# Kernel optimization log

Measured on AMD Instinct MI355X. Metric: run time of the kernel, lower is better.

## Reference

```python
import jax, jax.numpy as jnp
import numpy as np

N = 50000
E = 800000
H = 96
NUM_IN = 11
PE_DIM = 24
NUM_OUT = 1
NUM_LAYERS = 4
NUM_GRAPHS = 256


def _linear_params(key, d_in, d_out):
    k1, k2 = jax.random.split(key)
    bound = 1.0 / np.sqrt(d_in)
    w = jax.random.uniform(k1, (d_in, d_out), jnp.float32, -bound, bound)
    b = jax.random.uniform(k2, (d_out,), jnp.float32, -bound, bound)
    return w, b


def setup_inputs() -> dict:
    key = jax.random.key(0)
    ks = jax.random.split(key, 32)
    x = jax.random.normal(ks[0], (N, NUM_IN), jnp.float32)
    pos = jax.random.normal(ks[1], (N, 3), jnp.float32)
    pe = jax.random.normal(ks[2], (N, PE_DIM), jnp.float32)
    edge_index = jax.random.randint(ks[3], (2, E), 0, N, jnp.int64)
    batch = jnp.sort(jax.random.randint(ks[4], (N,), 0, NUM_GRAPHS, jnp.int64))
    embed_w1, embed_b1 = _linear_params(ks[5], NUM_IN + PE_DIM, H)
    embed_w2, embed_b2 = _linear_params(ks[6], H, H)
    # per-layer stacked params
    msg_w1 = []; msg_b1 = []; msg_w2 = []; msg_b2 = []
    upd_w1 = []; upd_b1 = []; upd_w2 = []; upd_b2 = []
    for l in range(NUM_LAYERS):
        w, b = _linear_params(ks[7 + l], 2 * H + 1, H); msg_w1.append(w); msg_b1.append(b)
        w, b = _linear_params(ks[11 + l], H, H); msg_w2.append(w); msg_b2.append(b)
        w, b = _linear_params(ks[15 + l], 2 * H, H); upd_w1.append(w); upd_b1.append(b)
        w, b = _linear_params(ks[19 + l], H, H); upd_w2.append(w); upd_b2.append(b)
    pre_w1, pre_b1 = _linear_params(ks[23], H, H)
    pre_w2, pre_b2 = _linear_params(ks[24], H, H)
    ro_w1, ro_b1 = _linear_params(ks[25], H, H)
    ro_w2, ro_b2 = _linear_params(ks[26], H, NUM_OUT)
    return {
        'x': x, 'pos': pos, 'pe': pe, 'edge_index': edge_index, 'batch': batch,
        'embed_w1': embed_w1, 'embed_b1': embed_b1, 'embed_w2': embed_w2, 'embed_b2': embed_b2,
        'msg_w1': jnp.stack(msg_w1), 'msg_b1': jnp.stack(msg_b1),
        'msg_w2': jnp.stack(msg_w2), 'msg_b2': jnp.stack(msg_b2),
        'upd_w1': jnp.stack(upd_w1), 'upd_b1': jnp.stack(upd_b1),
        'upd_w2': jnp.stack(upd_w2), 'upd_b2': jnp.stack(upd_b2),
        'pre_w1': pre_w1, 'pre_b1': pre_b1, 'pre_w2': pre_w2, 'pre_b2': pre_b2,
        'ro_w1': ro_w1, 'ro_b1': ro_b1, 'ro_w2': ro_w2, 'ro_b2': ro_b2,
    }


def _egnn_forward(x, pos, pe, edge_index, batch,
                  embed_w1, embed_b1, embed_w2, embed_b2,
                  msg_w1, msg_b1, msg_w2, msg_b2,
                  upd_w1, upd_b1, upd_w2, upd_b2,
                  pre_w1, pre_b1, pre_w2, pre_b2,
                  ro_w1, ro_b1, ro_w2, ro_b2):
    silu = jax.nn.silu
    send, rec = edge_index[0], edge_index[1]
    h = jnp.concatenate([x, pe], axis=-1)
    h = silu(h @ embed_w1 + embed_b1) @ embed_w2 + embed_b2  # [N,H]
    dist = jnp.linalg.norm(pos[send] - pos[rec], axis=1)[:, None]  # [E,1]
    for l in range(NUM_LAYERS):
        state = jnp.concatenate([h[send], h[rec], dist], axis=1)  # [E,2H+1]
        msg = silu(silu(state @ msg_w1[l] + msg_b1[l]) @ msg_w2[l] + msg_b2[l])  # [E,H]
        aggr = jax.ops.segment_sum(msg, rec, num_segments=h.shape[0])  # [N,H]
        upd_in = jnp.concatenate([h, aggr], axis=1)
        update = silu(upd_in @ upd_w1[l] + upd_b1[l]) @ upd_w2[l] + upd_b2[l]
        h = h + update
    h = silu(h @ pre_w1 + pre_b1) @ pre_w2 + pre_b2
    pooled = jax.ops.segment_sum(h, batch, num_segments=NUM_GRAPHS)  # [G,H]
    out = silu(pooled @ ro_w1 + ro_b1) @ ro_w2 + ro_b2  # [G,1]
    return jnp.squeeze(out)


def reference(x, pos, pe, edge_index, batch,
              embed_w1, embed_b1, embed_w2, embed_b2,
              msg_w1, msg_b1, msg_w2, msg_b2,
              upd_w1, upd_b1, upd_w2, upd_b2,
              pre_w1, pre_b1, pre_w2, pre_b2,
              ro_w1, ro_b1, ro_w2, ro_b2):
    return _egnn_forward(x, pos, pe, edge_index, batch,
                         embed_w1, embed_b1, embed_w2, embed_b2,
                         msg_w1, msg_b1, msg_w2, msg_b2,
                         upd_w1, upd_b1, upd_w2, upd_b2,
                         pre_w1, pre_b1, pre_w2, pre_b2,
                         ro_w1, ro_b1, ro_w2, ro_b2)
```

## Files before the change

### kernel.cpp

```cpp
#include <hip/hip_runtime.h>
#include <hip/hip_bf16.h>

#define HDIM 96
#define TILE 128
#define NTILE 64

typedef __attribute__((ext_vector_type(8))) short  short8;
typedef __attribute__((ext_vector_type(4))) short  short4v;
typedef __attribute__((ext_vector_type(4))) float  float4v;
typedef __attribute__((ext_vector_type(2))) float  float2v;
typedef __attribute__((ext_vector_type(4))) unsigned int uint4v;

static __device__ __forceinline__ short f2bf(float f){
    unsigned u = __float_as_uint(f);
    return (short)((u + 0x8000u) >> 16);
}
static __device__ __forceinline__ float bf2f(short s){
    unsigned u = ((unsigned)(unsigned short)s) << 16;
    return __uint_as_float(u);
}
static __device__ __forceinline__ float silu_f(float v){
    return v * __builtin_amdgcn_rcpf(1.0f + __expf(-v));
}

struct SwJob { const float* src; int ck; int ks; int ksrc; };
struct SwTable { SwJob j[22]; };

__global__ __launch_bounds__(256) void swizzle_all(SwTable T, const float* __restrict__ msg_w1,
                                                   short* __restrict__ dst, short* __restrict__ dst2,
                                                   int total1, int total2){
    int gid = blockIdx.x*256 + threadIdx.x;
    if (gid < total1) {
        int ksg = gid / 3072;
        int e   = gid % 3072;
        const float* src = T.j[0].src; int k0 = 0, ksrc = 0;
        #pragma unroll
        for (int jj = 0; jj < 22; ++jj){
            int s = T.j[jj].ck;
            if (ksg >= s && ksg < s + T.j[jj].ks){ src = T.j[jj].src; k0 = (ksg - s)*32; ksrc = T.j[jj].ksrc; }
        }
        int nt   = e >> 9;
        int rem  = e & 511;
        int lane = rem >> 3;
        int jx   = rem & 7;
        int k = k0 + ((lane >> 4) << 3) + jx;
        int f = nt*16 + (lane & 15);
        float v = (k < ksrc) ? src[(size_t)k*HDIM + f] : 0.0f;
        dst[gid] = f2bf(v);
    } else if (gid < total1 + total2) {
        int g2 = gid - total1;
        int layer = g2 / 18432;
        int e     = g2 % 18432;
        int ksg = e / 6144;
        int rem = e % 6144;
        int nt   = rem >> 9;
        int r2   = rem & 511;
        int lane = r2 >> 3;
        int jx   = r2 & 7;
        int k = ksg*32 + ((lane >> 4) << 3) + jx;
        int f = nt*16 + (lane & 15);
        int row = (f < 96) ? k : (96 + k);
        int col = (f < 96) ? f : (f - 96);
        dst2[g2] = f2bf(msg_w1[(size_t)layer*193*96 + (size_t)row*96 + col]);
    }
}

__global__ __launch_bounds__(256) void hist_kernel(const int* __restrict__ rec, int* __restrict__ deg, int E){
    int e = blockIdx.x*256 + threadIdx.x;
    if (e < E) atomicAdd(&deg[rec[e]], 1);
}

__global__ __launch_bounds__(256) void scan_part(const int* __restrict__ deg, int* __restrict__ part, int N){
    __shared__ int red[256];
    const int t = threadIdx.x;
    int base = blockIdx.x*1024;
    int s = 0;
    #pragma unroll
    for (int j=0;j<4;j++){ int i = base + j*256 + t; s += (i<N)?deg[i]:0; }
    red[t]=s; __syncthreads();
    #pragma unroll
    for (int off=128; off>0; off>>=1){ if (t<off) red[t]+=red[t+off]; __syncthreads(); }
    if (t==0) part[blockIdx.x]=red[0];
}
__global__ __launch_bounds__(256) void scan_top(int* __restrict__ part, int nb){
    __shared__ int buf[256];
    const int t = threadIdx.x;
    int v = (t < nb) ? part[t] : 0;
    buf[t] = v;
    __syncthreads();
    #pragma unroll
    for (int off=1; off<256; off<<=1){
        int u = (t>=off)?buf[t-off]:0;
        __syncthreads();
        buf[t] += u;
        __syncthreads();
    }
    if (t < nb) part[t] = buf[t] - v;
}
__global__ __launch_bounds__(256) void scan_final(const int* __restrict__ deg, const int* __restrict__ part,
                                                  int* __restrict__ cur, int N){
    __shared__ int tsum[256];
    const int t = threadIdx.x;
    int i0 = blockIdx.x*1024 + t*4;
    int a0 = (i0+0<N)?deg[i0+0]:0;
    int a1 = (i0+1<N)?deg[i0+1]:0;
    int a2 = (i0+2<N)?deg[i0+2]:0;
    int a3 = (i0+3<N)?deg[i0+3]:0;
    int s = a0+a1+a2+a3;
    tsum[t]=s; __syncthreads();
    #pragma unroll
    for (int off=1; off<256; off<<=1){
        int u = (t>=off)?tsum[t-off]:0;
        __syncthreads();
        tsum[t]+=u;
        __syncthreads();
    }
    int excl = tsum[t]-s + part[blockIdx.x];
    if (i0+0<N) cur[i0+0]=excl;
    if (i0+1<N) cur[i0+1]=excl+a0;
    if (i0+2<N) cur[i0+2]=excl+a0+a1;
    if (i0+3<N) cur[i0+3]=excl+a0+a1+a2;
}

__global__ __launch_bounds__(256) void scatter_kernel(
    const int* __restrict__ send, const int* __restrict__ rec, const float* __restrict__ pos,
    int* __restrict__ cur, int2* __restrict__ sd_s, int* __restrict__ rec_s, int E)
{
    int e = blockIdx.x*256 + threadIdx.x;
    if (e >= E) return;
    int s = send[e], r = rec[e];
    int p = atomicAdd(&cur[r], 1);
    float dx = pos[3*s]   - pos[3*r];
    float dy = pos[3*s+1] - pos[3*r+1];
    float dz = pos[3*s+2] - pos[3*r+2];
    float d = sqrtf(dx*dx + dy*dy + dz*dz);
    sd_s[p] = make_int2(s, __float_as_int(d));
    rec_s[p] = r;
}

__global__ __launch_bounds__(256,5) void edge_kernel(
    const short* __restrict__ SR,
    const int2* __restrict__ sd_s, const int* __restrict__ rec_s,
    const float* __restrict__ w1r192,
    const short* __restrict__ w2sw, const float* __restrict__ b2,
    float* __restrict__ aggr, float* __restrict__ stageA, float* __restrict__ stageB, int E)
{
    __shared__ short msgS[TILE*104];
    __shared__ int   recS[TILE];
    __shared__ int   startIdxS[TILE+1];
    __shared__ int   wcntS[2];
    const int t  = threadIdx.x;
    const int e0 = blockIdx.x * TILE;
    const int lane = t & 63;
    const int wv   = t >> 6;
    const int e_lo = wv * 32;
    const int col  = lane & 15;
    const int quad = lane >> 4;
    const int frow = quad * 4;
    const float4v fzero = {0.f,0.f,0.f,0.f};

    int se[2], re[2]; float dd[2];
    #pragma unroll
    for (int et=0; et<2; ++et){
        int ec = e0 + e_lo + et*16 + col; if (ec >= E) ec = E - 1;
        int2 sd = sd_s[ec];
        se[et] = sd.x; dd[et] = __int_as_float(sd.y);
        re[et] = rec_s[ec];
    }
    short8 Sv[2][3], Rv[2][3];
    #pragma unroll
    for (int et=0; et<2; ++et)
      #pragma unroll
      for (int ks=0; ks<3; ++ks){
        int f0 = ks*32 + quad*8;
        Sv[et][ks] = *(const short8*)(SR + (size_t)se[et]*192 + f0);
        Rv[et][ks] = *(const short8*)(SR + (size_t)re[et]*192 + 96 + f0);
      }

    int myRec = 0;
    bool flag = false;
    if (t < TILE) {
        int e = e0 + t; if (e >= E) e = E - 1;
        myRec = rec_s[e];
        recS[t] = myRec;
        int ep = e0 + t - 1; if (ep >= E) ep = E - 1;
        flag = (t == 0) || (myRec != rec_s[ep]);
    }
    unsigned long long bmask = __ballot(flag ? 1 : 0);
    int pre = __popcll(bmask & ((1ull << (t & 63)) - 1ull));
    if (t < TILE && (t & 63) == 0) wcntS[t >> 6] = __popcll(bmask);

    const bool firstB = (e0 > 0) && (rec_s[e0-1] == rec_s[e0]);
    const bool lastB  = (e0 + TILE < E) && (rec_s[e0 + TILE] == rec_s[(e0+TILE-1 < E)? e0+TILE-1 : E-1]);

    __syncthreads();

    if (flag) startIdxS[pre + ((t >> 6) ? wcntS[0] : 0)] = t;
    if (t == 0) startIdxS[wcntS[0] + wcntS[1]] = TILE;

    short8 frag[2][3];
    #pragma unroll
    for (int et=0; et<2; ++et){
        float d = dd[et];
        #pragma unroll
        for (int ks=0; ks<3; ++ks){
            int f0 = ks*32 + quad*8;
            float4v wa = *(const float4v*)(w1r192 + f0);
            float4v wb = *(const float4v*)(w1r192 + f0 + 4);
            short8 S8 = Sv[et][ks], R8 = Rv[et][ks];
            short8 fr;
            #pragma unroll
            for (int j=0;j<8;j++){
                float w = (j<4) ? wa[j] : wb[j-4];
                float v = bf2f(S8[j]) + bf2f(R8[j]) + d*w;
                fr[j] = f2bf(silu_f(v));
            }
            frag[et][ks] = fr;
        }
    }

    float4v acc2[2][6];
    #pragma unroll
    for (int i=0;i<2;i++)
      #pragma unroll
      for (int n=0;n<6;n++) acc2[i][n] = fzero;

    const short8* w2f = (const short8*)w2sw;
    #pragma unroll
    for (int ks = 0; ks < 3; ++ks) {
        #pragma unroll
        for (int mt = 0; mt < 6; ++mt) {
            short8 a = w2f[(ks*6+mt)*64 + lane];
            acc2[0][mt] = __builtin_amdgcn_mfma_f32_16x16x32_bf16(a, frag[0][ks], acc2[0][mt], 0, 0, 0);
            acc2[1][mt] = __builtin_amdgcn_mfma_f32_16x16x32_bf16(a, frag[1][ks], acc2[1][mt], 0, 0, 0);
        }
    }
    float4v b2v[6];
    #pragma unroll
    for (int mt=0; mt<6; ++mt) b2v[mt] = *(const float4v*)(b2 + mt*16 + frow);

    #pragma unroll
    for (int et=0; et<2; ++et){
        int e = e_lo + et*16 + col;
        bool valid = (e0 + e) < E;
        #pragma unroll
        for (int mt=0; mt<6; ++mt){
            short4v sv;
            #pragma unroll
            for (int r=0;r<4;r++){
                float u = silu_f(acc2[et][mt][r] + b2v[mt][r]);
                sv[r] = f2bf(valid ? u : 0.0f);
            }
            *(short4v*)(msgS + e*104 + mt*16 + frow) = sv;
        }
    }
    __syncthreads();

    const int nseg = wcntS[0] + wcntS[1];
    const int items = nseg * 12;
    for (int item = t; item < items; item += 256){
        int s  = item / 12;
        int fg = item - s*12;
        int r0 = startIdxS[s], r1 = startIdxS[s+1];
        float2v s01 = {0.f,0.f}, s23 = {0.f,0.f}, s45 = {0.f,0.f}, s67 = {0.f,0.f};
        for (int r = r0; r < r1; ++r){
            const unsigned* pp = (const unsigned*)(msgS + r*104 + fg*8);
            unsigned p0 = pp[0], p1 = pp[1], p2 = pp[2], p3 = pp[3];
            float2v a0 = { __uint_as_float(p0 << 16), __uint_as_float(p0 & 0xffff0000u) };
            float2v a1 = { __uint_as_float(p1 << 16), __uint_as_float(p1 & 0xffff0000u) };
            float2v a2 = { __uint_as_float(p2 << 16), __uint_as_float(p2 & 0xffff0000u) };
            float2v a3 = { __uint_as_float(p3 << 16), __uint_as_float(p3 & 0xffff0000u) };
            s01 += a0; s23 += a1; s45 += a2; s67 += a3;
        }
        int node = recS[r0];
        float* dstp;
        if (s == 0 && firstB)            dstp = stageB + (size_t)node*HDIM + fg*8;
        else if (s == nseg-1 && lastB)   dstp = stageA + (size_t)node*HDIM + fg*8;
        else                             dstp = aggr   + (size_t)node*HDIM + fg*8;
        float4v lo = {s01[0], s01[1], s23[0], s23[1]};
        float4v hi = {s45[0], s45[1], s67[0], s67[1]};
        *(float4v*)(dstp)     = lo;
        *(float4v*)(dstp + 4) = hi;
    }
}

__global__ __launch_bounds__(128,3) void update_kernel(
    short* __restrict__ hbf, const float* __restrict__ aggr,
    const float* __restrict__ stageA, const float* __restrict__ stageB,
    const int* __restrict__ deg, const int* __restrict__ cur,
    const short* __restrict__ w1sw, const float* __restrict__ b1,
    const short* __restrict__ w2sw, const float* __restrict__ b2,
    const short* __restrict__ w1sr_next, const float* __restrict__ msgb1_next,
    short* __restrict__ SR,
    const short* __restrict__ pw1, const float* __restrict__ pb1,
    const short* __restrict__ pw2, const float* __restrict__ pb2,
    const int* __restrict__ batch, float* __restrict__ pooled, int N)
{
    __shared__ short stateS[NTILE*208];
    __shared__ int   batchS[NTILE];
    __shared__ int   startIdxS[NTILE+1];
    __shared__ int   nsegS;
    const int t  = threadIdx.x;
    const int n0 = blockIdx.x * NTILE;

    #pragma unroll
    for (int it = 0; it < 12; ++it) {
        int q = it*128 + t;
        int c = q % 24;
        int i = q / 24;
        int node = n0 + i;
        if (c < 12) {
            uint4v v = {0u,0u,0u,0u};
            if (node < N) v = *(const uint4v*)(hbf + (size_t)node*HDIM + c*8);
            *(uint4v*)(stateS + i*200 + c*8) = v;
        } else {
            int cc = c - 12;
            short8 s8 = {0,0,0,0,0,0,0,0};
            if (node < N) {
                int dg = deg[node];
                int en = cur[node];
                int st = en - dg;
                bool bnd = (dg > 0) && (st/TILE != (en-1)/TILE);
                float4v a0, a1;
                if (bnd) {
                    size_t b = (size_t)node*HDIM + cc*8;
                    a0 = *(const float4v*)(stageA + b)     + *(const float4v*)(stageB + b);
                    a1 = *(const float4v*)(stageA + b + 4) + *(const float4v*)(stageB + b + 4);
                } else {
                    a0 = *(const float4v*)(aggr + (size_t)node*HDIM + cc*8);
                    a1 = *(const float4v*)(aggr + (size_t)node*HDIM + cc*8 + 4);
                }
                s8[0]=f2bf(a0[0]); s8[1]=f2bf(a0[1]); s8[2]=f2bf(a0[2]); s8[3]=f2bf(a0[3]);
                s8[4]=f2bf(a1[0]); s8[5]=f2bf(a1[1]); s8[6]=f2bf(a1[2]); s8[7]=f2bf(a1[3]);
            }
            *(short8*)(stateS + i*200 + HDIM + cc*8) = s8;
        }
    }
    __syncthreads();

    const int lane = t & 63;
    const int wv   = t >> 6;
    const int e_lo = wv * 32;
    const int col  = lane & 15;
    const int quad = lane >> 4;
    const int koff = quad * 8;
    const int frow = quad * 4;
    const float4v fzero = {0.f,0.f,0.f,0.f};

    float4v acc[2][6];
    #pragma unroll
    for (int i=0;i<2;i++)
      #pragma unroll
      for (int n=0;n<6;n++) acc[i][n] = fzero;

    const short8* w1f = (const short8*)w1sw;
    #pragma unroll
    for (int ks = 0; ks < 6; ++ks) {
        short8 bb0 = *(const short8*)(stateS + (e_lo+col)*200    + ks*32 + koff);
        short8 bb1 = *(const short8*)(stateS + (e_lo+16+col)*200 + ks*32 + koff);
        #pragma unroll
        for (int mt = 0; mt < 6; ++mt) {
            short8 a = w1f[(ks*6+mt)*64 + lane];
            acc[0][mt] = __builtin_amdgcn_mfma_f32_16x16x32_bf16(a, bb0, acc[0][mt], 0, 0, 0);
            acc[1][mt] = __builtin_amdgcn_mfma_f32_16x16x32_bf16(a, bb1, acc[1][mt], 0, 0, 0);
        }
    }
    float4v b1v[6];
    #pragma unroll
    for (int mt=0; mt<6; ++mt) b1v[mt] = *(const float4v*)(b1 + mt*16 + frow);
    __syncthreads();

    short* t1S = stateS;
    #pragma unroll
    for (int et=0; et<2; ++et){
        int e = e_lo + et*16 + col;
        #pragma unroll
        for (int mt=0; mt<6; ++mt){
            short4v sv;
            #pragma unroll
            for (int r=0;r<4;r++) sv[r] = f2bf(silu_f(acc[et][mt][r] + b1v[mt][r]));
            *(short4v*)(t1S + e*104 + mt*16 + frow) = sv;
        }
    }
    __syncthreads();

    float4v acc2[2][6];
    #pragma unroll
    for (int i=0;i<2;i++)
      #pragma unroll
      for (int n=0;n<6;n++) acc2[i][n] = fzero;

    const short8* w2f = (const short8*)w2sw;
    #pragma unroll
    for (int ks = 0; ks < 3; ++ks) {
        short8 bb0 = *(const short8*)(t1S + (e_lo+col)*104    + ks*32 + koff);
        short8 bb1 = *(const short8*)(t1S + (e_lo+16+col)*104 + ks*32 + koff);
        #pragma unroll
        for (int mt = 0; mt < 6; ++mt) {
            short8 a = w2f[(ks*6+mt)*64 + lane];
            acc2[0][mt] = __builtin_amdgcn_mfma_f32_16x16x32_bf16(a, bb0, acc2[0][mt], 0, 0, 0);
            acc2[1][mt] = __builtin_amdgcn_mfma_f32_16x16x32_bf16(a, bb1, acc2[1][mt], 0, 0, 0);
        }
    }
    float4v b2v[6];
    #pragma unroll
    for (int mt=0; mt<6; ++mt) b2v[mt] = *(const float4v*)(b2 + mt*16 + frow);
    __syncthreads();

    #pragma unroll
    for (int et=0; et<2; ++et){
        int erow = e_lo + et*16 + col;
        int node = n0 + erow;
        bool valid = node < N;
        size_t base = (size_t)node*HDIM;
        #pragma unroll
        for (int mt=0; mt<6; ++mt){
            int f0 = mt*16 + frow;
            short4v ov = {0,0,0,0};
            if (valid) ov = *(const short4v*)(hbf + base + f0);
            float4v o;
            #pragma unroll
            for (int r=0;r<4;r++) o[r] = bf2f(ov[r]) + acc2[et][mt][r] + b2v[mt][r];
            short4v sv = {f2bf(o[0]), f2bf(o[1]), f2bf(o[2]), f2bf(o[3])};
            if (valid) *(short4v*)(hbf + base + f0) = sv;
            *(short4v*)(stateS + erow*104 + f0) = sv;
        }
    }

    if (w1sr_next) {
        __syncthreads();
        float4v accS[2][12];
        #pragma unroll
        for (int i=0;i<2;i++)
          #pragma unroll
          for (int n=0;n<12;n++) accS[i][n] = fzero;

        const short8* wsf = (const short8*)w1sr_next;
        #pragma unroll
        for (int ks = 0; ks < 3; ++ks) {
            short8 bb0 = *(const short8*)(stateS + (e_lo+col)*104    + ks*32 + koff);
            short8 bb1 = *(const short8*)(stateS + (e_lo+16+col)*104 + ks*32 + koff);
            #pragma unroll
            for (int mt = 0; mt < 12; ++mt) {
                short8 a = wsf[(ks*12+mt)*64 + lane];
                accS[0][mt] = __builtin_amdgcn_mfma_f32_16x16x32_bf16(a, bb0, accS[0][mt], 0, 0, 0);
                accS[1][mt] = __builtin_amdgcn_mfma_f32_16x16x32_bf16(a, bb1, accS[1][mt], 0, 0, 0);
            }
        }
        float4v bnv[6];
        #pragma unroll
        for (int mt=0; mt<6; ++mt) bnv[mt] = *(const float4v*)(msgb1_next + mt*16 + frow);

        #pragma unroll
        for (int et=0; et<2; ++et){
            int node = n0 + e_lo + et*16 + col;
            if (node < N) {
                size_t sbase = (size_t)node*192;
                #pragma unroll
                for (int mt=0; mt<12; ++mt){
                    float4v o = accS[et][mt];
                    if (mt < 6) { o[0]+=bnv[mt][0]; o[1]+=bnv[mt][1]; o[2]+=bnv[mt][2]; o[3]+=bnv[mt][3]; }
                    short4v sv = {f2bf(o[0]), f2bf(o[1]), f2bf(o[2]), f2bf(o[3])};
                    *(short4v*)(SR + sbase + mt*16 + frow) = sv;
                }
            }
        }
    } else if (pw1) {
        if (t < NTILE) {
            int node = n0 + t;
            batchS[t] = batch[node < N ? node : N-1];
        }
        __syncthreads();

        bool flag = false;
        if (t < NTILE) flag = (t == 0) || (batchS[t] != batchS[t-1]);
        unsigned long long bm = __ballot(flag ? 1 : 0);
        if (t < NTILE) {
            int pre = __popcll(bm & ((1ull << t) - 1ull));
            if (flag) startIdxS[pre] = t;
            if (t == 0) nsegS = __popcll(bm);
        }

        float4v accp[2][6];
        #pragma unroll
        for (int i=0;i<2;i++)
          #pragma unroll
          for (int n=0;n<6;n++) accp[i][n] = fzero;

        const short8* pw1f = (const short8*)pw1;
        #pragma unroll
        for (int ks = 0; ks < 3; ++ks) {
            short8 bb0 = *(const short8*)(stateS + (e_lo+col)*104    + ks*32 + koff);
            short8 bb1 = *(const short8*)(stateS + (e_lo+16+col)*104 + ks*32 + koff);
            #pragma unroll
            for (int mt = 0; mt < 6; ++mt) {
                short8 a = pw1f[(ks*6+mt)*64 + lane];
                accp[0][mt] = __builtin_amdgcn_mfma_f32_16x16x32_bf16(a, bb0, accp[0][mt], 0, 0, 0);
                accp[1][mt] = __builtin_amdgcn_mfma_f32_16x16x32_bf16(a, bb1, accp[1][mt], 0, 0, 0);
            }
        }
        float4v pb1v[6];
        #pragma unroll
        for (int mt=0; mt<6; ++mt) pb1v[mt] = *(const float4v*)(pb1 + mt*16 + frow);

        short* t1p = stateS + NTILE*104;
        #pragma unroll
        for (int et=0; et<2; ++et){
            int e = e_lo + et*16 + col;
            #pragma unroll
            for (int mt=0; mt<6; ++mt){
                short4v sv;
                #pragma unroll
                for (int r=0;r<4;r++) sv[r] = f2bf(silu_f(accp[et][mt][r] + pb1v[mt][r]));
                *(short4v*)(t1p + e*104 + mt*16 + frow) = sv;
            }
        }
        __syncthreads();

        float4v accq[2][6];
        #pragma unroll
        for (int i=0;i<2;i++)
          #pragma unroll
          for (int n=0;n<6;n++) accq[i][n] = fzero;

        const short8* pw2f = (const short8*)pw2;
        #pragma unroll
        for (int ks = 0; ks < 3; ++ks) {
            short8 bb0 = *(const short8*)(t1p + (e_lo+col)*104    + ks*32 + koff);
            short8 bb1 = *(const short8*)(t1p + (e_lo+16+col)*104 + ks*32 + koff);
            #pragma unroll
            for (int mt = 0; mt < 6; ++mt) {
                short8 a = pw2f[(ks*6+mt)*64 + lane];
                accq[0][mt] = __builtin_amdgcn_mfma_f32_16x16x32_bf16(a, bb0, accq[0][mt], 0, 0, 0);
                accq[1][mt] = __builtin_amdgcn_mfma_f32_16x16x32_bf16(a, bb1, accq[1][mt], 0, 0, 0);
            }
        }
        float4v pb2v[6];
        #pragma unroll
        for (int mt=0; mt<6; ++mt) pb2v[mt] = *(const float4v*)(pb2 + mt*16 + frow);
        __syncthreads();

        float* msgS = (float*)stateS;
        #pragma unroll
        for (int et=0; et<2; ++et){
            int e = e_lo + et*16 + col;
            bool valid = (n0 + e) < N;
            #pragma unroll
            for (int mt=0; mt<6; ++mt){
                float4v v;
                #pragma unroll
                for (int r=0;r<4;r++){
                    float u = accq[et][mt][r] + pb2v[mt][r];
                    v[r] = valid ? u : 0.0f;
                }
                *(float4v*)(msgS + e*100 + mt*16 + frow) = v;
            }
        }
        __syncthreads();

        const int nseg = nsegS;
        if (t == 0) startIdxS[nseg] = NTILE;
        __syncthreads();

        const int items = nseg * 24;
        for (int item = t; item < items; item += 128){
            int s  = item / 24;
            int fg = item - s*24;
            int r0 = startIdxS[s], r1 = startIdxS[s+1];
            float4v sum = fzero;
            for (int r = r0; r < r1; ++r) sum += *(const float4v*)(msgS + r*100 + fg*4);
            float* dstp = pooled + (size_t)batchS[r0]*HDIM + fg*4;
            atomicAdd(dstp+0, sum[0]);
            atomicAdd(dstp+1, sum[1]);
            atomicAdd(dstp+2, sum[2]);
            atomicAdd(dstp+3, sum[3]);
        }
    }
}

__global__ __launch_bounds__(128,3) void embed_kernel(
    const float* __restrict__ x, const float* __restrict__ pe,
    const short* __restrict__ w1sw, const float* __restrict__ b1,
    const short* __restrict__ w2sw, const float* __restrict__ b2,
    short* __restrict__ hbf,
    const short* __restrict__ w1sr0, const float* __restrict__ msgb1_0,
    short* __restrict__ SR, int N)
{
    __shared__ short stateS[NTILE*72];
    __shared__ short t1S[NTILE*104];
    const int t  = threadIdx.x;
    const int n0 = blockIdx.x * NTILE;

    if (t < NTILE) {
        int node = n0 + t;
        short* row = stateS + t*72;
        if (node < N) {
            #pragma unroll
            for (int j=0;j<11;j++) row[j]    = f2bf(x[(size_t)node*11 + j]);
            #pragma unroll
            for (int j=0;j<24;j++) row[11+j] = f2bf(pe[(size_t)node*24 + j]);
            #pragma unroll
            for (int j=35;j<64;j++) row[j] = 0;
        } else {
            #pragma unroll
            for (int j=0;j<64;j++) row[j] = 0;
        }
    }
    __syncthreads();

    const int lane = t & 63;
    const int wv   = t >> 6;
    const int e_lo = wv * 32;
    const int col  = lane & 15;
    const int quad = lane >> 4;
    const int koff = quad * 8;
    const int frow = quad * 4;
    const float4v fzero = {0.f,0.f,0.f,0.f};

    float4v acc[2][6];
    #pragma unroll
    for (int i=0;i<2;i++)
      #pragma unroll
      for (int n=0;n<6;n++) acc[i][n] = fzero;

    const short8* w1f = (const short8*)w1sw;
    #pragma unroll
    for (int ks = 0; ks < 2; ++ks) {
        short8 bb0 = *(const short8*)(stateS + (e_lo+col)*72    + ks*32 + koff);
        short8 bb1 = *(const short8*)(stateS + (e_lo+16+col)*72 + ks*32 + koff);
        #pragma unroll
        for (int mt = 0; mt < 6; ++mt) {
            short8 a = w1f[(ks*6+mt)*64 + lane];
            acc[0][mt] = __builtin_amdgcn_mfma_f32_16x16x32_bf16(a, bb0, acc[0][mt], 0, 0, 0);
            acc[1][mt] = __builtin_amdgcn_mfma_f32_16x16x32_bf16(a, bb1, acc[1][mt], 0, 0, 0);
        }
    }
    float4v b1v[6];
    #pragma unroll
    for (int mt=0; mt<6; ++mt) b1v[mt] = *(const float4v*)(b1 + mt*16 + frow);

    #pragma unroll
    for (int et=0; et<2; ++et){
        int e = e_lo + et*16 + col;
        #pragma unroll
        for (int mt=0; mt<6; ++mt){
            short4v sv;
            #pragma unroll
            for (int r=0;r<4;r++) sv[r] = f2bf(silu_f(acc[et][mt][r] + b1v[mt][r]));
            *(short4v*)(t1S + e*104 + mt*16 + frow) = sv;
        }
    }
    __syncthreads();

    float4v acc2[2][6];
    #pragma unroll
    for (int i=0;i<2;i++)
      #pragma unroll
      for (int n=0;n<6;n++) acc2[i][n] = fzero;

    const short8* w2f = (const short8*)w2sw;
    #pragma unroll
    for (int ks = 0; ks < 3; ++ks) {
        short8 bb0 = *(const short8*)(t1S + (e_lo+col)*104    + ks*32 + koff);
        short8 bb1 = *(const short8*)(t1S + (e_lo+16+col)*104 + ks*32 + koff);
        #pragma unroll
        for (int mt = 0; mt < 6; ++mt) {
            short8 a = w2f[(ks*6+mt)*64 + lane];
            acc2[0][mt] = __builtin_amdgcn_mfma_f32_16x16x32_bf16(a, bb0, acc2[0][mt], 0, 0, 0);
            acc2[1][mt] = __builtin_amdgcn_mfma_f32_16x16x32_bf16(a, bb1, acc2[1][mt], 0, 0, 0);
        }
    }
    float4v b2v[6];
    #pragma unroll
    for (int mt=0; mt<6; ++mt) b2v[mt] = *(const float4v*)(b2 + mt*16 + frow);
    __syncthreads();

    #pragma unroll
    for (int et=0; et<2; ++et){
        int erow = e_lo + et*16 + col;
        int node = n0 + erow;
        bool valid = node < N;
        size_t base = (size_t)node*HDIM;
        #pragma unroll
        for (int mt=0; mt<6; ++mt){
            int f0 = mt*16 + frow;
            float4v o;
            #pragma unroll
            for (int r=0;r<4;r++) o[r] = acc2[et][mt][r] + b2v[mt][r];
            short4v sv = {f2bf(o[0]), f2bf(o[1]), f2bf(o[2]), f2bf(o[3])};
            if (valid) *(short4v*)(hbf + base + f0) = sv;
            *(short4v*)(t1S + erow*104 + f0) = sv;
        }
    }
    __syncthreads();

    float4v accS[2][12];
    #pragma unroll
    for (int i=0;i<2;i++)
      #pragma unroll
      for (int n=0;n<12;n++) accS[i][n] = fzero;

    const short8* wsf = (const short8*)w1sr0;
    #pragma unroll
    for (int ks = 0; ks < 3; ++ks) {
        short8 bb0 = *(const short8*)(t1S + (e_lo+col)*104    + ks*32 + koff);
        short8 bb1 = *(const short8*)(t1S + (e_lo+16+col)*104 + ks*32 + koff);
        #pragma unroll
        for (int mt = 0; mt < 12; ++mt) {
            short8 a = wsf[(ks*12+mt)*64 + lane];
            accS[0][mt] = __builtin_amdgcn_mfma_f32_16x16x32_bf16(a, bb0, accS[0][mt], 0, 0, 0);
            accS[1][mt] = __builtin_amdgcn_mfma_f32_16x16x32_bf16(a, bb1, accS[1][mt], 0, 0, 0);
        }
    }
    float4v bnv[6];
    #pragma unroll
    for (int mt=0; mt<6; ++mt) bnv[mt] = *(const float4v*)(msgb1_0 + mt*16 + frow);

    #pragma unroll
    for (int et=0; et<2; ++et){
        int node = n0 + e_lo + et*16 + col;
        if (node < N) {
            size_t sbase = (size_t)node*192;
            #pragma unroll
            for (int mt=0; mt<12; ++mt){
                float4v o = accS[et][mt];
                if (mt < 6) { o[0]+=bnv[mt][0]; o[1]+=bnv[mt][1]; o[2]+=bnv[mt][2]; o[3]+=bnv[mt][3]; }
                short4v sv = {f2bf(o[0]), f2bf(o[1]), f2bf(o[2]), f2bf(o[3])};
                *(short4v*)(SR + sbase + mt*16 + frow) = sv;
            }
        }
    }
}

__global__ __launch_bounds__(128) void readout_kernel(
    const float* __restrict__ pooled,
    const float* __restrict__ w1, const float* __restrict__ b1,
    const float* __restrict__ w2, const float* __restrict__ b2,
    float* __restrict__ out)
{
    __shared__ float red[128];
    const int g = blockIdx.x;
    const int t = threadIdx.x;
    float p = 0.0f;
    if (t < HDIM) {
        float acc = b1[t];
        for (int k = 0; k < HDIM; ++k)
            acc += pooled[(size_t)g*HDIM + k] * w1[(size_t)k*HDIM + t];
        acc = silu_f(acc);
        p = acc * w2[t];
    }
    red[t] = p;
    __syncthreads();
    for (int s = 64; s > 0; s >>= 1) {
        if (t < s) red[t] += red[t + s];
        __syncthreads();
    }
    if (t == 0) out[g] = red[0] + b2[0];
}

extern "C" void kernel_launch(void* const* d_in, const int* in_sizes, int n_in,
                              void* d_out, int out_size, void* d_ws, size_t ws_size,
                              hipStream_t stream)
{
    const float* x        = (const float*)d_in[0];
    const float* pos      = (const float*)d_in[1];
    const float* pe       = (const float*)d_in[2];
    const int*   ei       = (const int*)d_in[3];
    const int*   batch    = (const int*)d_in[4];
    const float* embed_w1 = (const float*)d_in[5];
    const float* embed_b1 = (const float*)d_in[6];
    const float* embed_w2 = (const float*)d_in[7];
    const float* embed_b2 = (const float*)d_in[8];
    const float* msg_w1   = (const float*)d_in[9];
    const float* msg_b1   = (const float*)d_in[10];
    const float* msg_w2   = (const float*)d_in[11];
    const float* msg_b2   = (const float*)d_in[12];
    const float* upd_w1   = (const float*)d_in[13];
    const float* upd_b1   = (const float*)d_in[14];
    const float* upd_w2   = (const float*)d_in[15];
    const float* upd_b2   = (const float*)d_in[16];
    const float* pre_w1   = (const float*)d_in[17];
    const float* pre_b1   = (const float*)d_in[18];
    const float* pre_w2   = (const float*)d_in[19];
    const float* pre_b2   = (const float*)d_in[20];
    const float* ro_w1    = (const float*)d_in[21];
    const float* ro_b1    = (const float*)d_in[22];
    const float* ro_w2    = (const float*)d_in[23];
    const float* ro_b2    = (const float*)d_in[24];

    const int E = in_sizes[3] / 2;
    const int N = in_sizes[4];
    const int G = out_size;

    char* ws = (char*)d_ws;
    size_t off = 0;
    auto alloc = [&](size_t bytes){ void* p = ws + off; off += (bytes + 255) & ~(size_t)255; return p; };
    short* hbf    = (short*)alloc((size_t)N*HDIM*2);
    float* aggr   = (float*)alloc((size_t)N*HDIM*4);
    float* stageA = (float*)alloc((size_t)N*HDIM*4);
    float* stageB = (float*)alloc((size_t)N*HDIM*4);
    float* pooled = (float*)alloc((size_t)G*HDIM*4);
    short* wsw    = (short*)alloc((size_t)59*3072*2);
    short* w1sr   = (short*)alloc((size_t)4*18432*2);
    short* SR     = (short*)alloc((size_t)N*192*2);
    int*   deg    = (int*)alloc((size_t)N*4);
    int*   cur    = (int*)alloc((size_t)N*4);
    int*   part   = (int*)alloc((size_t)256*4);
    int2*  sd_s   = (int2*)alloc((size_t)E*8);
    int*   rec_s  = (int*)alloc((size_t)E*4);

    hipMemsetAsync(aggr,   0, (size_t)N*HDIM*4, stream);
    hipMemsetAsync(pooled, 0, (size_t)G*HDIM*4, stream);
    hipMemsetAsync(deg,    0, (size_t)N*4, stream);

    SwTable T;
    for (int jj=0;jj<22;jj++){ T.j[jj].src = embed_w1; T.j[jj].ck = 1<<30; T.j[jj].ks = 0; T.j[jj].ksrc = 0; }
    int ck = 0, ji = 0;
    auto add = [&](const float* s, int ks, int ksrc){
        T.j[ji].src = s; T.j[ji].ck = ck; T.j[ji].ks = ks; T.j[ji].ksrc = ksrc;
        ji++; ck += ks;
    };
    add(embed_w1, 2, 35);
    add(embed_w2, 3, 96);
    add(pre_w1,   3, 96);
    add(pre_w2,   3, 96);
    for (int l=0;l<4;l++) add(msg_w2 + (size_t)l*96*96,  3, 96);
    for (int l=0;l<4;l++) add(upd_w1 + (size_t)l*192*96, 6, 192);
    for (int l=0;l<4;l++) add(upd_w2 + (size_t)l*96*96,  3, 96);
    const int total1 = 59*3072;
    const int total2 = 4*18432;
    swizzle_all<<<(total1+total2+255)/256, 256, 0, stream>>>(T, msg_w1, wsw, w1sr, total1, total2);

    const int nbE256 = (E + 255) / 256;
    const int nbScan = (N + 1023) / 1024;
    hist_kernel<<<nbE256, 256, 0, stream>>>(ei + E, deg, E);
    scan_part<<<nbScan, 256, 0, stream>>>(deg, part, N);
    scan_top<<<1, 256, 0, stream>>>(part, nbScan);
    scan_final<<<nbScan, 256, 0, stream>>>(deg, part, cur, N);
    scatter_kernel<<<nbE256, 256, 0, stream>>>(ei, ei + E, pos, cur, sd_s, rec_s, E);

    const int nbN = (N + NTILE - 1) / NTILE;
    embed_kernel<<<nbN, 128, 0, stream>>>(x, pe, wsw + 0, embed_b1, wsw + 2*3072, embed_b2,
                                          hbf, w1sr, msg_b1, SR, N);

    const int nbE = (E + TILE - 1) / TILE;
    for (int l = 0; l < 4; ++l) {
        edge_kernel<<<nbE, 256, 0, stream>>>(SR, sd_s, rec_s,
            msg_w1 + (size_t)l*193*96 + (size_t)192*96,
            wsw + (11 + 3*l)*3072, msg_b2 + l*96, aggr, stageA, stageB, E);
        const short* w1sr_next  = (l < 3) ? (w1sr + (size_t)(l+1)*18432) : nullptr;
        const float* msgb1_next = (l < 3) ? (msg_b1 + (l+1)*96) : nullptr;
        const short* pw1 = (l == 3) ? (wsw + 5*3072) : nullptr;
        const float* pb1 = (l == 3) ? pre_b1 : nullptr;
        const short* pw2 = (l == 3) ? (wsw + 8*3072) : nullptr;
        const float* pb2 = (l == 3) ? pre_b2 : nullptr;
        update_kernel<<<nbN, 128, 0, stream>>>(hbf, aggr, stageA, stageB, deg, cur,
            wsw + (23 + 6*l)*3072, upd_b1 + l*96,
            wsw + (47 + 3*l)*3072, upd_b2 + l*96,
            w1sr_next, msgb1_next, SR,
            pw1, pb1, pw2, pb2, batch, pooled, N);
    }

    readout_kernel<<<G, 128, 0, stream>>>(pooled, ro_w1, ro_b1, ro_w2, ro_b2, (float*)d_out);
}
```

Before: 748.7 us.

## Use four waves per node tile and shrink edge message LDS stride

The update and embed kernels now launch 256 threads per 64-node tile, so each wave handles 16 rows instead of 32. This halves the per-thread accumulator registers and doubles the parallelism per block. The edge kernel's message buffer stride drops from 104 to 100 shorts and its occupancy hint goes from 5 to 6 blocks, trading possible LDS bank conflicts for a smaller shared-memory footprint. Each wave now reloads the weight fragments for half as many rows, which lowers weight reuse.

Result: slower. 848.2 us (+13.3%).

```diff
diff --git a/kernel.cpp b/kernel.cpp
--- a/kernel.cpp
+++ b/kernel.cpp
@@ -138,14 +138,14 @@
     rec_s[p] = r;
 }
 
-__global__ __launch_bounds__(256,5) void edge_kernel(
+__global__ __launch_bounds__(256,6) void edge_kernel(
     const short* __restrict__ SR,
     const int2* __restrict__ sd_s, const int* __restrict__ rec_s,
     const float* __restrict__ w1r192,
     const short* __restrict__ w2sw, const float* __restrict__ b2,
     float* __restrict__ aggr, float* __restrict__ stageA, float* __restrict__ stageB, int E)
 {
-    __shared__ short msgS[TILE*104];
+    __shared__ short msgS[TILE*100];
     __shared__ int   recS[TILE];
     __shared__ int   startIdxS[TILE+1];
     __shared__ int   wcntS[2];
@@ -251,7 +251,7 @@
                 float u = silu_f(acc2[et][mt][r] + b2v[mt][r]);
                 sv[r] = f2bf(valid ? u : 0.0f);
             }
-            *(short4v*)(msgS + e*104 + mt*16 + frow) = sv;
+            *(short4v*)(msgS + e*100 + mt*16 + frow) = sv;
         }
     }
     __syncthreads();
@@ -264,7 +264,7 @@
         int r0 = startIdxS[s], r1 = startIdxS[s+1];
         float2v s01 = {0.f,0.f}, s23 = {0.f,0.f}, s45 = {0.f,0.f}, s67 = {0.f,0.f};
         for (int r = r0; r < r1; ++r){
-            const unsigned* pp = (const unsigned*)(msgS + r*104 + fg*8);
+            const unsigned* pp = (const unsigned*)(msgS + r*100 + fg*8);
             unsigned p0 = pp[0], p1 = pp[1], p2 = pp[2], p3 = pp[3];
             float2v a0 = { __uint_as_float(p0 << 16), __uint_as_float(p0 & 0xffff0000u) };
             float2v a1 = { __uint_as_float(p1 << 16), __uint_as_float(p1 & 0xffff0000u) };
@@ -284,7 +284,7 @@
     }
 }
 
-__global__ __launch_bounds__(128,3) void update_kernel(
+__global__ __launch_bounds__(256,3) void update_kernel(
     short* __restrict__ hbf, const float* __restrict__ aggr,
     const float* __restrict__ stageA, const float* __restrict__ stageB,
     const int* __restrict__ deg, const int* __restrict__ cur,
@@ -304,8 +304,8 @@
     const int n0 = blockIdx.x * NTILE;
 
     #pragma unroll
-    for (int it = 0; it < 12; ++it) {
-        int q = it*128 + t;
+    for (int it = 0; it < 6; ++it) {
+        int q = it*256 + t;
         int c = q % 24;
         int i = q / 24;
         int node = n0 + i;
@@ -340,29 +340,25 @@
 
     const int lane = t & 63;
     const int wv   = t >> 6;
-    const int e_lo = wv * 32;
+    const int rb   = wv * 16;
     const int col  = lane & 15;
     const int quad = lane >> 4;
     const int koff = quad * 8;
     const int frow = quad * 4;
     const float4v fzero = {0.f,0.f,0.f,0.f};
 
-    float4v acc[2][6];
-    #pragma unroll
-    for (int i=0;i<2;i++)
-      #pragma unroll
-      for (int n=0;n<6;n++) acc[i][n] = fzero;
+    float4v acc[6];
+    #pragma unroll
+    for (int n=0;n<6;n++) acc[n] = fzero;
 
     const short8* w1f = (const short8*)w1sw;
     #pragma unroll
     for (int ks = 0; ks < 6; ++ks) {
-        short8 bb0 = *(const short8*)(stateS + (e_lo+col)*200    + ks*32 + koff);
-        short8 bb1 = *(const short8*)(stateS + (e_lo+16+col)*200 + ks*32 + koff);
+        short8 bb = *(const short8*)(stateS + (rb+col)*200 + ks*32 + koff);
         #pragma unroll
         for (int mt = 0; mt < 6; ++mt) {
             short8 a = w1f[(ks*6+mt)*64 + lane];
-            acc[0][mt] = __builtin_amdgcn_mfma_f32_16x16x32_bf16(a, bb0, acc[0][mt], 0, 0, 0);
-            acc[1][mt] = __builtin_amdgcn_mfma_f32_16x16x32_bf16(a, bb1, acc[1][mt], 0, 0, 0);
+            acc[mt] = __builtin_amdgcn_mfma_f32_16x16x32_bf16(a, bb, acc[mt], 0, 0, 0);
         }
     }
     float4v b1v[6];
@@ -371,35 +367,30 @@
     __syncthreads();
 
     short* t1S = stateS;
-    #pragma unroll
-    for (int et=0; et<2; ++et){
-        int e = e_lo + et*16 + col;
+    {
+        int e = rb + col;
         #pragma unroll
         for (int mt=0; mt<6; ++mt){
             short4v sv;
             #pragma unroll
-            for (int r=0;r<4;r++) sv[r] = f2bf(silu_f(acc[et][mt][r] + b1v[mt][r]));
+            for (int r=0;r<4;r++) sv[r] = f2bf(silu_f(acc[mt][r] + b1v[mt][r]));
             *(short4v*)(t1S + e*104 + mt*16 + frow) = sv;
         }
     }
     __syncthreads();
 
-    float4v acc2[2][6];
-    #pragma unroll
-    for (int i=0;i<2;i++)
-      #pragma unroll
-      for (int n=0;n<6;n++) acc2[i][n] = fzero;
+    float4v acc2[6];
+    #pragma unroll
+    for (int n=0;n<6;n++) acc2[n] = fzero;
 
     const short8* w2f = (const short8*)w2sw;
     #pragma unroll
     for (int ks = 0; ks < 3; ++ks) {
-        short8 bb0 = *(const short8*)(t1S + (e_lo+col)*104    + ks*32 + koff);
-        short8 bb1 = *(const short8*)(t1S + (e_lo+16+col)*104 + ks*32 + koff);
+        short8 bb = *(const short8*)(t1S + (rb+col)*104 + ks*32 + koff);
         #pragma unroll
         for (int mt = 0; mt < 6; ++mt) {
             short8 a = w2f[(ks*6+mt)*64 + lane];
-            acc2[0][mt] = __builtin_amdgcn_mfma_f32_16x16x32_bf16(a, bb0, acc2[0][mt], 0, 0, 0);
-            acc2[1][mt] = __builtin_amdgcn_mfma_f32_16x16x32_bf16(a, bb1, acc2[1][mt], 0, 0, 0);
+            acc2[mt] = __builtin_amdgcn_mfma_f32_16x16x32_bf16(a, bb, acc2[mt], 0, 0, 0);
         }
     }
     float4v b2v[6];
@@ -407,9 +398,8 @@
     for (int mt=0; mt<6; ++mt) b2v[mt] = *(const float4v*)(b2 + mt*16 + frow);
     __syncthreads();
 
-    #pragma unroll
-    for (int et=0; et<2; ++et){
-        int erow = e_lo + et*16 + col;
+    {
+        int erow = rb + col;
         int node = n0 + erow;
         bool valid = node < N;
         size_t base = (size_t)node*HDIM;
@@ -420,7 +410,7 @@
             if (valid) ov = *(const short4v*)(hbf + base + f0);
             float4v o;
             #pragma unroll
-            for (int r=0;r<4;r++) o[r] = bf2f(ov[r]) + acc2[et][mt][r] + b2v[mt][r];
+            for (int r=0;r<4;r++) o[r] = bf2f(ov[r]) + acc2[mt][r] + b2v[mt][r];
             short4v sv = {f2bf(o[0]), f2bf(o[1]), f2bf(o[2]), f2bf(o[3])};
             if (valid) *(short4v*)(hbf + base + f0) = sv;
             *(short4v*)(stateS + erow*104 + f0) = sv;
@@ -429,36 +419,31 @@
 
     if (w1sr_next) {
         __syncthreads();
-        float4v accS[2][12];
-        #pragma unroll
-        for (int i=0;i<2;i++)
-          #pragma unroll
-          for (int n=0;n<12;n++) accS[i][n] = fzero;
+        float4v accS[12];
+        #pragma unroll
+        for (int n=0;n<12;n++) accS[n] = fzero;
 
         const short8* wsf = (const short8*)w1sr_next;
         #pragma unroll
         for (int ks = 0; ks < 3; ++ks) {
-            short8 bb0 = *(const short8*)(stateS + (e_lo+col)*104    + ks*32 + koff);
-            short8 bb1 = *(const short8*)(stateS + (e_lo+16+col)*104 + ks*32 + koff);
+            short8 bb = *(const short8*)(stateS + (rb+col)*104 + ks*32 + koff);
             #pragma unroll
             for (int mt = 0; mt < 12; ++mt) {
                 short8 a = wsf[(ks*12+mt)*64 + lane];
-                accS[0][mt] = __builtin_amdgcn_mfma_f32_16x16x32_bf16(a, bb0, accS[0][mt], 0, 0, 0);
-                accS[1][mt] = __builtin_amdgcn_mfma_f32_16x16x32_bf16(a, bb1, accS[1][mt], 0, 0, 0);
+                accS[mt] = __builtin_amdgcn_mfma_f32_16x16x32_bf16(a, bb, accS[mt], 0, 0, 0);
             }
         }
         float4v bnv[6];
         #pragma unroll
         for (int mt=0; mt<6; ++mt) bnv[mt] = *(const float4v*)(msgb1_next + mt*16 + frow);
 
-        #pragma unroll
-        for (int et=0; et<2; ++et){
-            int node = n0 + e_lo + et*16 + col;
+        {
+            int node = n0 + rb + col;
             if (node < N) {
                 size_t sbase = (size_t)node*192;
                 #pragma unroll
                 for (int mt=0; mt<12; ++mt){
-                    float4v o = accS[et][mt];
+                    float4v o = accS[mt];
                     if (mt < 6) { o[0]+=bnv[mt][0]; o[1]+=bnv[mt][1]; o[2]+=bnv[mt][2]; o[3]+=bnv[mt][3]; }
                     short4v sv = {f2bf(o[0]), f2bf(o[1]), f2bf(o[2]), f2bf(o[3])};
                     *(short4v*)(SR + sbase + mt*16 + frow) = sv;
@@ -481,22 +466,18 @@
             if (t == 0) nsegS = __popcll(bm);
         }
 
-        float4v accp[2][6];
-        #pragma unroll
-        for (int i=0;i<2;i++)
-          #pragma unroll
-          for (int n=0;n<6;n++) accp[i][n] = fzero;
+        float4v accp[6];
+        #pragma unroll
+        for (int n=0;n<6;n++) accp[n] = fzero;
 
         const short8* pw1f = (const short8*)pw1;
         #pragma unroll
         for (int ks = 0; ks < 3; ++ks) {
-            short8 bb0 = *(const short8*)(stateS + (e_lo+col)*104    + ks*32 + koff);
-            short8 bb1 = *(const short8*)(stateS + (e_lo+16+col)*104 + ks*32 + koff);
+            short8 bb = *(const short8*)(stateS + (rb+col)*104 + ks*32 + koff);
             #pragma unroll
             for (int mt = 0; mt < 6; ++mt) {
                 short8 a = pw1f[(ks*6+mt)*64 + lane];
-                accp[0][mt] = __builtin_amdgcn_mfma_f32_16x16x32_bf16(a, bb0, accp[0][mt], 0, 0, 0);
-                accp[1][mt] = __builtin_amdgcn_mfma_f32_16x16x32_bf16(a, bb1, accp[1][mt], 0, 0, 0);
+                accp[mt] = __builtin_amdgcn_mfma_f32_16x16x32_bf16(a, bb, accp[mt], 0, 0, 0);
             }
         }
         float4v pb1v[6];
@@ -504,35 +485,30 @@
         for (int mt=0; mt<6; ++mt) pb1v[mt] = *(const float4v*)(pb1 + mt*16 + frow);
 
         short* t1p = stateS + NTILE*104;
-        #pragma unroll
-        for (int et=0; et<2; ++et){
-            int e = e_lo + et*16 + col;
+        {
+            int e = rb + col;
             #pragma unroll
             for (int mt=0; mt<6; ++mt){
                 short4v sv;
                 #pragma unroll
-                for (int r=0;r<4;r++) sv[r] = f2bf(silu_f(accp[et][mt][r] + pb1v[mt][r]));
+                for (int r=0;r<4;r++) sv[r] = f2bf(silu_f(accp[mt][r] + pb1v[mt][r]));
                 *(short4v*)(t1p + e*104 + mt*16 + frow) = sv;
             }
         }
         __syncthreads();
 
-        float4v accq[2][6];
-        #pragma unroll
-        for (int i=0;i<2;i++)
-          #pragma unroll
-          for (int n=0;n<6;n++) accq[i][n] = fzero;
+        float4v accq[6];
+        #pragma unroll
+        for (int n=0;n<6;n++) accq[n] = fzero;
 
         const short8* pw2f = (const short8*)pw2;
         #pragma unroll
         for (int ks = 0; ks < 3; ++ks) {
-            short8 bb0 = *(const short8*)(t1p + (e_lo+col)*104    + ks*32 + koff);
-            short8 bb1 = *(const short8*)(t1p + (e_lo+16+col)*104 + ks*32 + koff);
+            short8 bb = *(const short8*)(t1p + (rb+col)*104 + ks*32 + koff);
             #pragma unroll
             for (int mt = 0; mt < 6; ++mt) {
                 short8 a = pw2f[(ks*6+mt)*64 + lane];
-                accq[0][mt] = __builtin_amdgcn_mfma_f32_16x16x32_bf16(a, bb0, accq[0][mt], 0, 0, 0);
-                accq[1][mt] = __builtin_amdgcn_mfma_f32_16x16x32_bf16(a, bb1, accq[1][mt], 0, 0, 0);
+                accq[mt] = __builtin_amdgcn_mfma_f32_16x16x32_bf16(a, bb, accq[mt], 0, 0, 0);
             }
         }
         float4v pb2v[6];
@@ -541,16 +517,15 @@
         __syncthreads();
 
         float* msgS = (float*)stateS;
-        #pragma unroll
-        for (int et=0; et<2; ++et){
-            int e = e_lo + et*16 + col;
+        {
+            int e = rb + col;
             bool valid = (n0 + e) < N;
             #pragma unroll
             for (int mt=0; mt<6; ++mt){
                 float4v v;
                 #pragma unroll
                 for (int r=0;r<4;r++){
-                    float u = accq[et][mt][r] + pb2v[mt][r];
+                    float u = accq[mt][r] + pb2v[mt][r];
                     v[r] = valid ? u : 0.0f;
                 }
                 *(float4v*)(msgS + e*100 + mt*16 + frow) = v;
@@ -563,7 +538,7 @@
         __syncthreads();
 
         const int items = nseg * 24;
-        for (int item = t; item < items; item += 128){
+        for (int item = t; item < items; item += 256){
             int s  = item / 24;
             int fg = item - s*24;
             int r0 = startIdxS[s], r1 = startIdxS[s+1];
@@ -578,7 +553,7 @@
     }
 }
 
-__global__ __launch_bounds__(128,3) void embed_kernel(
+__global__ __launch_bounds__(256,3) void embed_kernel(
     const float* __restrict__ x, const float* __restrict__ pe,
     const short* __restrict__ w1sw, const float* __restrict__ b1,
     const short* __restrict__ w2sw, const float* __restrict__ b2,
@@ -610,64 +585,55 @@
 
     const int lane = t & 63;
     const int wv   = t >> 6;
-    const int e_lo = wv * 32;
+    const int rb   = wv * 16;
     const int col  = lane & 15;
     const int quad = lane >> 4;
     const int koff = quad * 8;
     const int frow = quad * 4;
     const float4v fzero = {0.f,0.f,0.f,0.f};
 
-    float4v acc[2][6];
-    #pragma unroll
-    for (int i=0;i<2;i++)
-      #pragma unroll
-      for (int n=0;n<6;n++) acc[i][n] = fzero;
+    float4v acc[6];
+    #pragma unroll
+    for (int n=0;n<6;n++) acc[n] = fzero;
 
     const short8* w1f = (const short8*)w1sw;
     #pragma unroll
     for (int ks = 0; ks < 2; ++ks) {
-        short8 bb0 = *(const short8*)(stateS + (e_lo+col)*72    + ks*32 + koff);
-        short8 bb1 = *(const short8*)(stateS + (e_lo+16+col)*72 + ks*32 + koff);
+        short8 bb = *(const short8*)(stateS + (rb+col)*72 + ks*32 + koff);
         #pragma unroll
         for (int mt = 0; mt < 6; ++mt) {
             short8 a = w1f[(ks*6+mt)*64 + lane];
-            acc[0][mt] = __builtin_amdgcn_mfma_f32_16x16x32_bf16(a, bb0, acc[0][mt], 0, 0, 0);
-            acc[1][mt] = __builtin_amdgcn_mfma_f32_16x16x32_bf16(a, bb1, acc[1][mt], 0, 0, 0);
+            acc[mt] = __builtin_amdgcn_mfma_f32_16x16x32_bf16(a, bb, acc[mt], 0, 0, 0);
         }
     }
     float4v b1v[6];
     #pragma unroll
     for (int mt=0; mt<6; ++mt) b1v[mt] = *(const float4v*)(b1 + mt*16 + frow);
 
-    #pragma unroll
-    for (int et=0; et<2; ++et){
-        int e = e_lo + et*16 + col;
+    {
+        int e = rb + col;
         #pragma unroll
         for (int mt=0; mt<6; ++mt){
             short4v sv;
             #pragma unroll
-            for (int r=0;r<4;r++) sv[r] = f2bf(silu_f(acc[et][mt][r] + b1v[mt][r]));
+            for (int r=0;r<4;r++) sv[r] = f2bf(silu_f(acc[mt][r] + b1v[mt][r]));
             *(short4v*)(t1S + e*104 + mt*16 + frow) = sv;
         }
     }
     __syncthreads();
 
-    float4v acc2[2][6];
-    #pragma unroll
-    for (int i=0;i<2;i++)
-      #pragma unroll
-      for (int n=0;n<6;n++) acc2[i][n] = fzero;
+    float4v acc2[6];
+    #pragma unroll
+    for (int n=0;n<6;n++) acc2[n] = fzero;
 
     const short8* w2f = (const short8*)w2sw;
     #pragma unroll
     for (int ks = 0; ks < 3; ++ks) {
-        short8 bb0 = *(const short8*)(t1S + (e_lo+col)*104    + ks*32 + koff);
-        short8 bb1 = *(const short8*)(t1S + (e_lo+16+col)*104 + ks*32 + koff);
+        short8 bb = *(const short8*)(t1S + (rb+col)*104 + ks*32 + koff);
         #pragma unroll
         for (int mt = 0; mt < 6; ++mt) {
             short8 a = w2f[(ks*6+mt)*64 + lane];
-            acc2[0][mt] = __builtin_amdgcn_mfma_f32_16x16x32_bf16(a, bb0, acc2[0][mt], 0, 0, 0);
-            acc2[1][mt] = __builtin_amdgcn_mfma_f32_16x16x32_bf16(a, bb1, acc2[1][mt], 0, 0, 0);
+            acc2[mt] = __builtin_amdgcn_mfma_f32_16x16x32_bf16(a, bb, acc2[mt], 0, 0, 0);
         }
     }
     float4v b2v[6];
@@ -675,9 +641,8 @@
     for (int mt=0; mt<6; ++mt) b2v[mt] = *(const float4v*)(b2 + mt*16 + frow);
     __syncthreads();
 
-    #pragma unroll
-    for (int et=0; et<2; ++et){
-        int erow = e_lo + et*16 + col;
+    {
+        int erow = rb + col;
         int node = n0 + erow;
         bool valid = node < N;
         size_t base = (size_t)node*HDIM;
@@ -686,7 +651,7 @@
             int f0 = mt*16 + frow;
             float4v o;
             #pragma unroll
-            for (int r=0;r<4;r++) o[r] = acc2[et][mt][r] + b2v[mt][r];
+            for (int r=0;r<4;r++) o[r] = acc2[mt][r] + b2v[mt][r];
             short4v sv = {f2bf(o[0]), f2bf(o[1]), f2bf(o[2]), f2bf(o[3])};
             if (valid) *(short4v*)(hbf + base + f0) = sv;
             *(short4v*)(t1S + erow*104 + f0) = sv;
@@ -694,36 +659,31 @@
     }
     __syncthreads();
 
-    float4v accS[2][12];
-    #pragma unroll
-    for (int i=0;i<2;i++)
-      #pragma unroll
-      for (int n=0;n<12;n++) accS[i][n] = fzero;
+    float4v accS[12];
+    #pragma unroll
+    for (int n=0;n<12;n++) accS[n] = fzero;
 
     const short8* wsf = (const short8*)w1sr0;
     #pragma unroll
     for (int ks = 0; ks < 3; ++ks) {
-        short8 bb0 = *(const short8*)(t1S + (e_lo+col)*104    + ks*32 + koff);
-        short8 bb1 = *(const short8*)(t1S + (e_lo+16+col)*104 + ks*32 + koff);
+        short8 bb = *(const short8*)(t1S + (rb+col)*104 + ks*32 + koff);
         #pragma unroll
         for (int mt = 0; mt < 12; ++mt) {
             short8 a = wsf[(ks*12+mt)*64 + lane];
-            accS[0][mt] = __builtin_amdgcn_mfma_f32_16x16x32_bf16(a, bb0, accS[0][mt], 0, 0, 0);
-            accS[1][mt] = __builtin_amdgcn_mfma_f32_16x16x32_bf16(a, bb1, accS[1][mt], 0, 0, 0);
+            accS[mt] = __builtin_amdgcn_mfma_f32_16x16x32_bf16(a, bb, accS[mt], 0, 0, 0);
         }
     }
     float4v bnv[6];
     #pragma unroll
     for (int mt=0; mt<6; ++mt) bnv[mt] = *(const float4v*)(msgb1_0 + mt*16 + frow);
 
-    #pragma unroll
-    for (int et=0; et<2; ++et){
-        int node = n0 + e_lo + et*16 + col;
+    {
+        int node = n0 + rb + col;
         if (node < N) {
             size_t sbase = (size_t)node*192;
             #pragma unroll
             for (int mt=0; mt<12; ++mt){
-                float4v o = accS[et][mt];
+                float4v o = accS[mt];
                 if (mt < 6) { o[0]+=bnv[mt][0]; o[1]+=bnv[mt][1]; o[2]+=bnv[mt][2]; o[3]+=bnv[mt][3]; }
                 short4v sv = {f2bf(o[0]), f2bf(o[1]), f2bf(o[2]), f2bf(o[3])};
                 *(short4v*)(SR + sbase + mt*16 + frow) = sv;
@@ -840,7 +800,7 @@
     scatter_kernel<<<nbE256, 256, 0, stream>>>(ei, ei + E, pos, cur, sd_s, rec_s, E);
 
     const int nbN = (N + NTILE - 1) / NTILE;
-    embed_kernel<<<nbN, 128, 0, stream>>>(x, pe, wsw + 0, embed_b1, wsw + 2*3072, embed_b2,
+    embed_kernel<<<nbN, 256, 0, stream>>>(x, pe, wsw + 0, embed_b1, wsw + 2*3072, embed_b2,
                                           hbf, w1sr, msg_b1, SR, N);
 
     const int nbE = (E + TILE - 1) / TILE;
@@ -854,7 +814,7 @@
         const float* pb1 = (l == 3) ? pre_b1 : nullptr;
         const short* pw2 = (l == 3) ? (wsw + 8*3072) : nullptr;
         const float* pb2 = (l == 3) ? pre_b2 : nullptr;
-        update_kernel<<<nbN, 128, 0, stream>>>(hbf, aggr, stageA, stageB, deg, cur,
+        update_kernel<<<nbN, 256, 0, stream>>>(hbf, aggr, stageA, stageB, deg, cur,
             wsw + (23 + 6*l)*3072, upd_b1 + l*96,
             wsw + (47 + 3*l)*3072, upd_b2 + l*96,
             w1sr_next, msgb1_next, SR,
```
